# Kernel tuning notes

Measured on AMD Instinct MI355X. Metric: run time of the kernel, lower is better.

Reference implementation:

```python
import jax, jax.numpy as jnp
import numpy as np

LN_EPS = 1e-12


def setup_inputs() -> dict:
    key = jax.random.key(0)
    ks = jax.random.split(key, 5)
    B, N, D_IN, D_OUT, E = 32, 2048, 128, 128, 64
    return {
        "x": jax.random.normal(ks[0], (B, N, D_IN), dtype=jnp.float32),
        "node_embeddings": jax.random.normal(ks[1], (N, E), dtype=jnp.float32),
        "time_embeddings": jax.random.normal(ks[2], (E,), dtype=jnp.float32),
        "weights_pool": jax.random.normal(ks[3], (E, 2, D_IN, D_OUT), dtype=jnp.float32) * 0.02,
        "bias_pool": jax.random.normal(ks[4], (E, D_OUT), dtype=jnp.float32) * 0.02,
        "ln_weight": jnp.ones((E,), dtype=jnp.float32),
        "ln_bias": jnp.zeros((E,), dtype=jnp.float32),
    }


def reference(x, node_embeddings, time_embeddings, weights_pool, bias_pool, ln_weight, ln_bias):
    # e: [N, E] = LayerNorm(node_emb + time_emb)  (dropout in eval mode = identity)
    e = node_embeddings + time_embeddings[None, :]
    mu = jnp.mean(e, axis=-1, keepdims=True)
    var = jnp.mean(jnp.square(e - mu), axis=-1, keepdims=True)
    e = (e - mu) * jax.lax.rsqrt(var + LN_EPS) * ln_weight + ln_bias

    # adaptive adjacency: softmax over rows of e @ e.T  -> [N, N]
    adj = jax.nn.softmax(jnp.einsum('nd,md->nm', e, e), axis=1)

    # per-node weights [N, 2, I, O] and bias [N, O]
    weights = jnp.einsum('nd,dkio->nkio', e, weights_pool)
    bias = e @ bias_pool  # [N, O]

    # supports: k=0 identity (x itself), k=1 adjacency aggregation
    x_agg = jnp.einsum('nm,bmc->bnc', adj, x)        # [B, N, I]
    x_g = jnp.stack([x, x_agg], axis=2)              # [B, N, 2, I]

    # per-node batched GEMM + bias
    out = jnp.einsum('bnki,nkio->bno', x_g, weights) + bias
    return out
```

## Files before the change

kernel.cpp:

```cpp
#include <hip/hip_runtime.h>


typedef unsigned short u16;
typedef unsigned int u32;
typedef __attribute__((ext_vector_type(8))) short bf16x8;
typedef __attribute__((ext_vector_type(4))) float f32x4;
typedef const __attribute__((address_space(1))) u16* gas1;
typedef __attribute__((address_space(3))) u16* las3;

#define NN 2048
#define EE 64
#define CC 128
#define BB 32

__device__ __forceinline__ u16 f2bf(float f) {
  u32 u = __builtin_bit_cast(u32, f);
  u += 0x7fffu + ((u >> 16) & 1u);
  return (u16)(u >> 16);
}

__device__ __forceinline__ f32x4 mfma16(bf16x8 a, bf16x8 b, f32x4 c) {
  return __builtin_amdgcn_mfma_f32_16x16x32_bf16(a, b, c, 0, 0, 0);
}

__global__ __launch_bounds__(256) void k_mega0(
    const float* __restrict__ x, const float* __restrict__ ne,
    const float* __restrict__ te, const float* __restrict__ pool,
    const float* __restrict__ bias_pool, const float* __restrict__ lnw,
    const float* __restrict__ lnb,
    float* __restrict__ e, u16* __restrict__ e_bf, float* __restrict__ bias_out,
    u16* __restrict__ pool_r, u16* __restrict__ x_t, u16* __restrict__ xg_t) {
  __shared__ __align__(16) char smem[34048];
  int bid = blockIdx.x;
  int tid = threadIdx.x;
  if (bid < 512) {
    float* sh = (float*)smem;
    int nw = tid >> 6, d = tid & 63;
    int n = bid * 4 + nw;
    float v = ne[n * EE + d] + te[d];
    float s = v;
#pragma unroll
    for (int off = 32; off > 0; off >>= 1) s += __shfl_xor(s, off);
    float mean = s * (1.0f / 64.0f);
    float c = v - mean;
    float q = c * c;
#pragma unroll
    for (int off = 32; off > 0; off >>= 1) q += __shfl_xor(q, off);
    float inv = rsqrtf(q * (1.0f / 64.0f) + 1e-12f);
    float ev = c * inv * lnw[d] + lnb[d];
    e[n * EE + d] = ev;
    e_bf[n * EE + d] = f2bf(ev);
    sh[nw * 64 + d] = ev;
    __syncthreads();
#pragma unroll
    for (int oo = 0; oo < 2; ++oo) {
      int o = oo * 64 + d;
      float acc = 0.f;
#pragma unroll 8
      for (int dd = 0; dd < 64; ++dd) acc += sh[nw * 64 + dd] * bias_pool[dd * CC + o];
      bias_out[n * CC + o] = acc;
    }
  } else if (bid < 768) {
    float* t = (float*)smem;
    int ki = bid - 512;
    for (int it = 0; it < 32; ++it) {
      int idx = it * 256 + tid;
      int d = idx >> 7, o = idx & 127;
      t[o * 65 + d] = pool[d * 32768 + ki * 128 + o];
    }
    __syncthreads();
    for (int it = 0; it < 32; ++it) {
      int idx = it * 256 + tid;
      int o = idx >> 6, d = idx & 63;
      pool_r[((size_t)o * 256 + ki) * 64 + d] = f2bf(t[o * 65 + d]);
    }
  } else {
    u16* t = (u16*)smem;
    int bx = bid - 768;
    int b = bx >> 5;
    int m0 = (bx & 31) * 64;
    for (int it = 0; it < 32; ++it) {
      int idx = it * 256 + tid;
      int m = idx >> 7, c = idx & 127;
      float v = x[((size_t)b * NN + m0 + m) * CC + c];
      t[c * 68 + m] = f2bf(v);
    }
    __syncthreads();
    for (int it = 0; it < 32; ++it) {
      int idx = it * 256 + tid;
      int c = idx >> 6, m = idx & 63;
      x_t[((size_t)b * CC + c) * NN + m0 + m] = t[c * 68 + m];
    }
    for (int it = 0; it < 16; ++it) {
      int idx = it * 256 + tid;
      int m = idx >> 6, c2 = idx & 63;
      float2 v = *(const float2*)&x[((size_t)b * NN + m0 + m) * CC + c2 * 2];
      u32 pk = (u32)f2bf(v.x) | ((u32)f2bf(v.y) << 16);
      *(u32*)&xg_t[(((size_t)(m0 + m)) * 32 + b) * 256 + c2 * 2] = pk;
    }
  }
}

__global__ __launch_bounds__(256) void k_Sexp(const float* __restrict__ e,
                                              u16* __restrict__ P,
                                              float* __restrict__ rs) {
  __shared__ float er[64 * 68];
  __shared__ float ec[64 * 68];
  int n0 = (blockIdx.x >> 5) * 64, m0 = (blockIdx.x & 31) * 64;
  int tid = threadIdx.x;
  for (int it = 0; it < 16; ++it) {
    int idx = it * 256 + tid;
    int r = idx >> 6, d = idx & 63;
    er[r * 68 + d] = e[(n0 + r) * EE + d];
    ec[r * 68 + d] = e[(m0 + r) * EE + d];
  }
  __syncthreads();
  int tx = tid & 15, ty = tid >> 4;
  float acc[4][4] = {};
  for (int d4 = 0; d4 < 64; d4 += 4) {
    f32x4 av[4], bv[4];
#pragma unroll
    for (int i = 0; i < 4; ++i) av[i] = *(const f32x4*)&er[(ty + 16 * i) * 68 + d4];
#pragma unroll
    for (int j = 0; j < 4; ++j) bv[j] = *(const f32x4*)&ec[(tx + 16 * j) * 68 + d4];
#pragma unroll
    for (int i = 0; i < 4; ++i)
#pragma unroll
      for (int j = 0; j < 4; ++j) {
        acc[i][j] += av[i][0] * bv[j][0];
        acc[i][j] += av[i][1] * bv[j][1];
        acc[i][j] += av[i][2] * bv[j][2];
        acc[i][j] += av[i][3] * bv[j][3];
      }
  }
#pragma unroll
  for (int i = 0; i < 4; ++i) {
    float s = 0.f;
#pragma unroll
    for (int j = 0; j < 4; ++j) {
      float pv = __expf(acc[i][j]);
      P[(size_t)(n0 + ty + 16 * i) * NN + m0 + tx + 16 * j] = f2bf(pv);
      s += pv;
    }
#pragma unroll
    for (int off = 8; off > 0; off >>= 1) s += __shfl_xor(s, off);
    if (tx == 0) atomicAdd(&rs[n0 + ty + 16 * i], s);
  }
}

__global__ __launch_bounds__(256, 4) void k_mega2(
    const u16* __restrict__ P, const u16* __restrict__ x_t,
    const float* __restrict__ rs, u16* __restrict__ xg_t,
    const u16* __restrict__ e_bf, const u16* __restrict__ pool_r,
    u16* __restrict__ W_p) {
  __shared__ __align__(16) char smem[34048];
  int tid = threadIdx.x;
  int lane = tid & 63, w = tid >> 6;
  int lm = lane & 15, lq = lane >> 4;
  if (blockIdx.x < 512) {
    u16* As = (u16*)smem;
    u16* Bs = (u16*)(smem + 16384);
    int mb = blockIdx.x & 15, b = blockIdx.x >> 4;
    int n0 = mb * 128;
    int wm = w >> 1, wn = w & 1;
    f32x4 acc[4][4] = {};
    const u16* a_src = P + (size_t)n0 * NN;
    const u16* b_src = x_t + (size_t)b * CC * NN;
    for (int kc = 0; kc < NN; kc += 64) {
      __syncthreads();
#pragma unroll
      for (int ii = 0; ii < 4; ++ii) {
        int idx = ii * 256 + tid;
        int row = idx >> 3, ch = idx & 7;
        int sc = kc + ((ch ^ (row & 7)) << 3);
        __builtin_amdgcn_global_load_lds((gas1)(a_src + (size_t)row * NN + sc),
                                         (las3)(As + (size_t)(ii * 256 + w * 64) * 8), 16, 0, 0);
        __builtin_amdgcn_global_load_lds((gas1)(b_src + (size_t)row * NN + sc),
                                         (las3)(Bs + (size_t)(ii * 256 + w * 64) * 8), 16, 0, 0);
      }
      __syncthreads();
#pragma unroll
      for (int kk = 0; kk < 64; kk += 32) {
        int cb = (kk >> 3) + lq;
        bf16x8 af[4], bq[4];
#pragma unroll
        for (int i = 0; i < 4; ++i) {
          int row = wm * 64 + i * 16 + lm;
          af[i] = *(const bf16x8*)&As[row * 64 + ((cb ^ (row & 7)) << 3)];
        }
#pragma unroll
        for (int j = 0; j < 4; ++j) {
          int row = wn * 64 + j * 16 + lm;
          bq[j] = *(const bf16x8*)&Bs[row * 64 + ((cb ^ (row & 7)) << 3)];
        }
#pragma unroll
        for (int i = 0; i < 4; ++i)
#pragma unroll
          for (int j = 0; j < 4; ++j)
            acc[i][j] = mfma16(af[i], bq[j], acc[i][j]);
      }
    }
#pragma unroll
    for (int i = 0; i < 4; ++i) {
      int nr = n0 + wm * 64 + i * 16 + lq * 4;
#pragma unroll
      for (int r = 0; r < 4; ++r) {
        float sc = 1.0f / rs[nr + r];
#pragma unroll
        for (int j = 0; j < 4; ++j) {
          int c = wn * 64 + j * 16 + lm;
          xg_t[((size_t)(nr + r) * 32 + b) * 256 + 128 + c] = f2bf(acc[i][j][r] * sc);
        }
      }
    }
  } else {
    u16* Tl = (u16*)smem;
    int g = blockIdx.x - 512;
    int og = g >> 7, ng = g & 127;
    int o0 = og * 4, n0 = ng * 16;
    bf16x8 eB[2];
#pragma unroll
    for (int ks = 0; ks < 2; ++ks)
      eB[ks] = *(const bf16x8*)&e_bf[(n0 + lm) * EE + ks * 32 + lq * 8];
    const u16* pbase = pool_r + (size_t)(o0 + w) * 256 * 64;
#pragma unroll
    for (int ct = 0; ct < 16; ++ct) {
      const u16* ap = pbase + (ct * 16 + lm) * 64 + lq * 8;
      bf16x8 pA0 = *(const bf16x8*)ap;
      bf16x8 pA1 = *(const bf16x8*)(ap + 32);
      f32x4 gv = {0.f, 0.f, 0.f, 0.f};
      gv = mfma16(pA0, eB[0], gv);
      gv = mfma16(pA1, eB[1], gv);
      ushort4 h;
      h.x = f2bf(gv[0]); h.y = f2bf(gv[1]); h.z = f2bf(gv[2]); h.w = f2bf(gv[3]);
      *(ushort4*)&Tl[w * 4232 + lm * 264 + ct * 16 + lq * 4] = h;
    }
    __syncthreads();
#pragma unroll
    for (int it = 0; it < 8; ++it) {
      int idx = it * 256 + tid;
      int n = idx >> 7, rem = idx & 127;
      int ks = rem >> 4, rem2 = rem & 15;
      int o = rem2 >> 2, ki8 = rem2 & 3;
      uint4 v = *(const uint4*)&Tl[o * 4232 + n * 264 + ks * 32 + ki8 * 8];
      *(uint4*)&W_p[(size_t)(n0 + n) * 32768 + ks * 4096 + (o0 + o) * 32 + ki8 * 8] = v;
    }
  }
}

__global__ __launch_bounds__(256, 3) void k_apply(const u16* __restrict__ xg_t,
                                                  const u16* __restrict__ W_p,
                                                  const float* __restrict__ bias,
                                                  float* __restrict__ out) {
  int n0 = blockIdx.x * 2;
  int tid = threadIdx.x;
  int lane = tid & 63, w = tid >> 6;
  int lm = lane & 15, lq = lane >> 4;
  int n = n0 + (w & 1), oh = w >> 1;
  const u16* xb = xg_t + (size_t)n * 32 * 256;
  const u16* wb = W_p + (size_t)n * 32768 + (size_t)oh * 64 * 32;
  f32x4 acc[2][4] = {};
#pragma unroll
  for (int ks = 0; ks < 8; ++ks) {
    int ko = ks * 32 + lq * 8;
    bf16x8 a0 = *(const bf16x8*)&xb[lm * 256 + ko];
    bf16x8 a1 = *(const bf16x8*)&xb[(16 + lm) * 256 + ko];
#pragma unroll
    for (int ot = 0; ot < 4; ++ot) {
      bf16x8 bv = *(const bf16x8*)&wb[(size_t)ks * 4096 + (ot * 16 + lm) * 32 + lq * 8];
      acc[0][ot] = mfma16(a0, bv, acc[0][ot]);
      acc[1][ot] = mfma16(a1, bv, acc[1][ot]);
    }
  }
#pragma unroll
  for (int ot = 0; ot < 4; ++ot) {
    int oc = oh * 64 + ot * 16 + lm;
    float bv = bias[n * CC + oc];
#pragma unroll
    for (int mt = 0; mt < 2; ++mt)
#pragma unroll
      for (int r = 0; r < 4; ++r) {
        int b = mt * 16 + lq * 4 + r;
        out[((size_t)b * NN + n) * CC + oc] = acc[mt][ot][r] + bv;
      }
  }
}

extern "C" void kernel_launch(void* const* d_in, const int* in_sizes, int n_in,
                              void* d_out, int out_size, void* d_ws, size_t ws_size,
                              hipStream_t stream) {
  const float* x        = (const float*)d_in[0];
  const float* node_emb = (const float*)d_in[1];
  const float* time_emb = (const float*)d_in[2];
  const float* pool     = (const float*)d_in[3];
  const float* bias_pl  = (const float*)d_in[4];
  const float* ln_w     = (const float*)d_in[5];
  const float* ln_b     = (const float*)d_in[6];
  float* out = (float*)d_out;

  char* p = (char*)d_ws;
  auto alloc = [&](size_t bytes) {
    char* r = p;
    p += (bytes + 255) & ~(size_t)255;
    return r;
  };
  float* e      = (float*)alloc((size_t)NN * EE * 4);
  u16*   e_bf   = (u16*)  alloc((size_t)NN * EE * 2);
  float* biasb  = (float*)alloc((size_t)NN * CC * 4);
  u16*   Pm     = (u16*)  alloc((size_t)NN * NN * 2);
  float* rs     = (float*)alloc((size_t)NN * 4);
  u16*   x_t    = (u16*)  alloc((size_t)BB * CC * NN * 2);
  u16*   xg_t   = (u16*)  alloc((size_t)NN * BB * 256 * 2);
  u16*   pool_r = (u16*)  alloc((size_t)128 * 256 * 64 * 2);
  u16*   W_p    = (u16*)  alloc((size_t)NN * 32768 * 2);

  if (ws_size < (size_t)(p - (char*)d_ws)) return;

  (void)hipMemsetAsync(rs, 0, (size_t)NN * 4, stream);

  k_mega0<<<1792, 256, 0, stream>>>(x, node_emb, time_emb, pool, bias_pl, ln_w, ln_b,
                                    e, e_bf, biasb, pool_r, x_t, xg_t);
  k_Sexp<<<1024, 256, 0, stream>>>(e, Pm, rs);
  k_mega2<<<4608, 256, 0, stream>>>(Pm, x_t, rs, xg_t, e_bf, pool_r, W_p);
  k_apply<<<NN / 2, 256, 0, stream>>>(xg_t, W_p, biasb, out);
}
```

Before: 257.4 us.

## Fuse xg_t packing into transpose pass and retile per-node weight generation

The x prep block now writes the packed bf16 xg_t entries from the same load used for the transpose, exchanging neighbouring values with a lane shuffle. This removes the second global read of x. The weight-generation branch switches from 4 outputs × 16 nodes per block to 2 outputs × 32 nodes, with each warp covering half of the ki range. This reuses each loaded pool_r fragment across two node tiles, raising MFMA reuse and cutting pool_r reads. The new mapping changes the LDS layout and the store pattern to W_p, which now writes narrower contiguous segments per node.

```diff
diff --git a/kernel.cpp b/kernel.cpp
--- a/kernel.cpp
+++ b/kernel.cpp
@@ -83,20 +83,19 @@
       int idx = it * 256 + tid;
       int m = idx >> 7, c = idx & 127;
       float v = x[((size_t)b * NN + m0 + m) * CC + c];
-      t[c * 68 + m] = f2bf(v);
+      u16 bf = f2bf(v);
+      t[c * 68 + m] = bf;
+      int partner = __shfl_xor((int)bf, 1);
+      if ((c & 1) == 0) {
+        u32 pk = (u32)bf | ((u32)partner << 16);
+        *(u32*)&xg_t[(((size_t)(m0 + m)) * 32 + b) * 256 + c] = pk;
+      }
     }
     __syncthreads();
     for (int it = 0; it < 32; ++it) {
       int idx = it * 256 + tid;
       int c = idx >> 6, m = idx & 63;
       x_t[((size_t)b * CC + c) * NN + m0 + m] = t[c * 68 + m];
-    }
-    for (int it = 0; it < 16; ++it) {
-      int idx = it * 256 + tid;
-      int m = idx >> 6, c2 = idx & 63;
-      float2 v = *(const float2*)&x[((size_t)b * NN + m0 + m) * CC + c2 * 2];
-      u32 pk = (u32)f2bf(v.x) | ((u32)f2bf(v.y) << 16);
-      *(u32*)&xg_t[(((size_t)(m0 + m)) * 32 + b) * 256 + c2 * 2] = pk;
     }
   }
 }
@@ -216,33 +215,39 @@
   } else {
     u16* Tl = (u16*)smem;
     int g = blockIdx.x - 512;
-    int og = g >> 7, ng = g & 127;
-    int o0 = og * 4, n0 = ng * 16;
-    bf16x8 eB[2];
-#pragma unroll
-    for (int ks = 0; ks < 2; ++ks)
-      eB[ks] = *(const bf16x8*)&e_bf[(n0 + lm) * EE + ks * 32 + lq * 8];
-    const u16* pbase = pool_r + (size_t)(o0 + w) * 256 * 64;
-#pragma unroll
-    for (int ct = 0; ct < 16; ++ct) {
+    int og = g & 63, nb = g >> 6;
+    int o0 = og * 2, n0 = nb * 32;
+    int o_l = w & 1, kih = w >> 1;
+    bf16x8 eB[2][2];
+#pragma unroll
+    for (int nt = 0; nt < 2; ++nt)
+#pragma unroll
+      for (int ks = 0; ks < 2; ++ks)
+        eB[nt][ks] = *(const bf16x8*)&e_bf[(n0 + nt * 16 + lm) * EE + ks * 32 + lq * 8];
+    const u16* pbase = pool_r + ((size_t)(o0 + o_l) * 256 + kih * 128) * 64;
+#pragma unroll
+    for (int ct = 0; ct < 8; ++ct) {
       const u16* ap = pbase + (ct * 16 + lm) * 64 + lq * 8;
       bf16x8 pA0 = *(const bf16x8*)ap;
       bf16x8 pA1 = *(const bf16x8*)(ap + 32);
-      f32x4 gv = {0.f, 0.f, 0.f, 0.f};
-      gv = mfma16(pA0, eB[0], gv);
-      gv = mfma16(pA1, eB[1], gv);
-      ushort4 h;
-      h.x = f2bf(gv[0]); h.y = f2bf(gv[1]); h.z = f2bf(gv[2]); h.w = f2bf(gv[3]);
-      *(ushort4*)&Tl[w * 4232 + lm * 264 + ct * 16 + lq * 4] = h;
+#pragma unroll
+      for (int nt = 0; nt < 2; ++nt) {
+        f32x4 gv = {0.f, 0.f, 0.f, 0.f};
+        gv = mfma16(pA0, eB[nt][0], gv);
+        gv = mfma16(pA1, eB[nt][1], gv);
+        ushort4 h;
+        h.x = f2bf(gv[0]); h.y = f2bf(gv[1]); h.z = f2bf(gv[2]); h.w = f2bf(gv[3]);
+        *(ushort4*)&Tl[o_l * 8456 + (nt * 16 + lm) * 264 + kih * 128 + ct * 16 + lq * 4] = h;
+      }
     }
     __syncthreads();
 #pragma unroll
     for (int it = 0; it < 8; ++it) {
       int idx = it * 256 + tid;
-      int n = idx >> 7, rem = idx & 127;
-      int ks = rem >> 4, rem2 = rem & 15;
+      int n = idx >> 6, rem = idx & 63;
+      int ks = rem >> 3, rem2 = rem & 7;
       int o = rem2 >> 2, ki8 = rem2 & 3;
-      uint4 v = *(const uint4*)&Tl[o * 4232 + n * 264 + ks * 32 + ki8 * 8];
+      uint4 v = *(const uint4*)&Tl[o * 8456 + n * 264 + ks * 32 + ki8 * 8];
       *(uint4*)&W_p[(size_t)(n0 + n) * 32768 + ks * 4096 + (o0 + o) * 32 + ki8 * 8] = v;
     }
   }
```

After: 251.5 us. 1.02x faster.
